# Performance work log

Measured on AMD Instinct MI355X. Metric: run time of the kernel, lower is better.

Reference implementation:

```python
import jax, jax.numpy as jnp
import numpy as np

NUM_HEADS = 16
THETA = 10000.0


def _rope_headaxis(x, cos, sin):
    # x: (B, T, H, D). Faithful to the source module: RoPE angles are
    # indexed by the HEAD axis (the module's view_as_complex bug), with
    # consecutive pairs along D forming (real, imag).
    B, T, H, D = x.shape
    xp = x.reshape(B, T, H, D // 2, 2)
    x0, x1 = xp[..., 0], xp[..., 1]
    # cos/sin: (H, D//2) broadcast over (B, T)
    o0 = x0 * cos - x1 * sin
    o1 = x0 * sin + x1 * cos
    return jnp.stack([o0, o1], axis=-1).reshape(B, T, H, D)


def setup_inputs() -> dict:
    key = jax.random.key(0)
    k1, k2, k3 = jax.random.split(key, 3)
    B, T, C = 2, 2048, 1024
    H = NUM_HEADS
    D = C // H
    KV = 2 * 2048  # kv_seq_len * 2 cache allocation
    x = jax.random.normal(k1, (B, T, C), dtype=jnp.float32)
    w_qkv = jax.random.normal(k2, (3 * C, C), dtype=jnp.float32) * 0.02
    w_out = jax.random.normal(k3, (C, C), dtype=jnp.float32) * 0.02
    cache_k = jnp.zeros((B, KV, H, D), dtype=jnp.float32)
    cache_v = jnp.zeros((B, KV, H, D), dtype=jnp.float32)
    return {"x": x, "w_qkv": w_qkv, "w_out": w_out,
            "cache_k": cache_k, "cache_v": cache_v, "start_pos": 0}


def reference(x, w_qkv, w_out, cache_k, cache_v, start_pos):
    B, T, C = x.shape
    H = NUM_HEADS
    D = C // H
    scale = 1.0 / np.sqrt(D).astype(np.float32)

    qkv = x @ w_qkv.T  # (B, T, 3C)
    q, k, v = jnp.split(qkv, 3, axis=-1)
    q = q.reshape(B, T, H, D)
    k = k.reshape(B, T, H, D)
    v = v.reshape(B, T, H, D)

    # RoPE angles: outer(arange(T), inv_freq) sliced to first H rows
    # (source applies positions along the head axis).
    dim_half = D // 2
    inv_freq = 1.0 / (THETA ** (jnp.arange(dim_half, dtype=jnp.float32) / dim_half))
    angles = jnp.arange(H, dtype=jnp.float32)[:, None] * inv_freq[None, :]  # (H, D/2)
    cos, sin = jnp.cos(angles), jnp.sin(angles)
    q = _rope_headaxis(q, cos, sin)
    k = _rope_headaxis(k, cos, sin)

    end_pos = start_pos + T
    cache_k = cache_k.at[:, start_pos:end_pos].set(jax.lax.stop_gradient(k))
    cache_v = cache_v.at[:, start_pos:end_pos].set(jax.lax.stop_gradient(v))
    k_full = cache_k[:, :end_pos]  # (B, S, H, D)
    v_full = cache_v[:, :end_pos]

    scores = jnp.einsum('bthd,bshd->bhts', q, k_full) * scale  # (B,H,T,S)
    causal = jnp.triu(jnp.ones((T, end_pos), dtype=bool), k=1)
    scores = jnp.where(causal[None, None], -jnp.inf, scores)
    probs = jax.nn.softmax(scores, axis=-1)  # dropout is identity at inference
    ctx = jnp.einsum('bhts,bshd->bthd', probs, v_full).reshape(B, T, C)
    return ctx @ w_out.T
```

## Files before the change

### kernel.cpp

```cpp
#include <hip/hip_runtime.h>
#include <hip/hip_bf16.h>
#include <stdint.h>

typedef __attribute__((ext_vector_type(8))) short short8;
typedef __attribute__((ext_vector_type(4))) float f32x4;

static __device__ __forceinline__ unsigned short f2bf(float f) {
  union { float f; unsigned u; } v; v.f = f;
  return (unsigned short)((v.u + 0x7fffu + ((v.u >> 16) & 1u)) >> 16);
}
static __device__ __forceinline__ float bf2f(unsigned short h) {
  union { unsigned u; float f; } v; v.u = ((unsigned)h) << 16;
  return v.f;
}
static __device__ __forceinline__ unsigned cvt_pk_bf16(float lo, float hi) {
  unsigned r;
  asm("v_cvt_pk_bf16_f32 %0, %1, %2" : "=v"(r) : "v"(lo), "v"(hi));
  return r;
}

#define GLL16(gp, lp) __builtin_amdgcn_global_load_lds(                        \
    (__attribute__((address_space(1))) void*)(uintptr_t)(gp),                  \
    (__attribute__((address_space(3))) void*)(lp), 16, 0, 0)

#define SWZ(r, e) ((e) ^ (((r) & 7) << 3))

__global__ void cast3(const float* __restrict__ a, unsigned short* __restrict__ oa, int na4,
                      const float* __restrict__ b, unsigned short* __restrict__ ob, int nb4,
                      const float* __restrict__ c, unsigned short* __restrict__ oc, int nc4) {
  int i = blockIdx.x * 256 + threadIdx.x;
  const float* src;
  unsigned short* dst;
  int j = i;
  if (j < na4) { src = a; dst = oa; }
  else if ((j -= na4) < nb4) { src = b; dst = ob; }
  else { j -= nb4; if (j >= nc4) return; src = c; dst = oc; }
  const float4 v = reinterpret_cast<const float4*>(src)[j];
  ushort4 o;
  o.x = f2bf(v.x); o.y = f2bf(v.y); o.z = f2bf(v.z); o.w = f2bf(v.w);
  reinterpret_cast<ushort4*>(dst)[j] = o;
}

__global__ __launch_bounds__(256) void gemm_qkv(
    const unsigned short* __restrict__ A, const unsigned short* __restrict__ B,
    unsigned short* __restrict__ qb, unsigned short* __restrict__ kb,
    unsigned short* __restrict__ vt) {
  constexpr int K = 1024;
  __shared__ unsigned short smem[128 * 136];
  const int tid = threadIdx.x;
  const int lane = tid & 63;
  const int w = tid >> 6;
  const int wr = w >> 1, wc = w & 1;
  const int l15 = lane & 15, lg = lane >> 4;
  const size_t bm = (size_t)blockIdx.x * 128;
  const size_t bn = (size_t)blockIdx.y * 128;
  const unsigned short* Ab = A + bm * K;
  const unsigned short* Bb = B + bn * K;
  f32x4 acc[4][4];
#pragma unroll
  for (int m = 0; m < 4; ++m)
#pragma unroll
    for (int n = 0; n < 4; ++n) acc[m][n] = (f32x4){0.f, 0.f, 0.f, 0.f};

#pragma unroll
  for (int p = 0; p < 2; ++p) {
    const int flat = p * 256 + tid;
    const int row = flat >> 2;
    const int c8 = (flat & 3) << 3;
    GLL16(Ab + (size_t)row * K + c8, smem + flat * 8);
    GLL16(Bb + (size_t)row * K + c8, smem + 8192 + flat * 8);
  }
  __syncthreads();
  int cur = 0;
  for (int k0 = 0; k0 < K; k0 += 32) {
    if (k0 + 32 < K) {
      const int nb = cur ^ 1;
#pragma unroll
      for (int p = 0; p < 2; ++p) {
        const int flat = p * 256 + tid;
        const int row = flat >> 2;
        const int c8 = (flat & 3) << 3;
        GLL16(Ab + (size_t)row * K + k0 + 32 + c8, smem + nb * 4096 + flat * 8);
        GLL16(Bb + (size_t)row * K + k0 + 32 + c8, smem + 8192 + nb * 4096 + flat * 8);
      }
    }
    const unsigned short* Asc = smem + cur * 4096;
    const unsigned short* Bsc = smem + 8192 + cur * 4096;
    short8 af[4], bf[4];
#pragma unroll
    for (int m = 0; m < 4; ++m)
      af[m] = *reinterpret_cast<const short8*>(Asc + ((wr * 64 + m * 16 + l15) * 32 + lg * 8));
#pragma unroll
    for (int n = 0; n < 4; ++n)
      bf[n] = *reinterpret_cast<const short8*>(Bsc + ((wc * 64 + n * 16 + l15) * 32 + lg * 8));
#pragma unroll
    for (int m = 0; m < 4; ++m)
#pragma unroll
      for (int n = 0; n < 4; ++n)
        acc[m][n] = __builtin_amdgcn_mfma_f32_16x16x32_bf16(af[m], bf[n], acc[m][n], 0, 0, 0);
    __syncthreads();
    cur ^= 1;
  }

  const int sec = (int)(bn >> 10);
  const int hbase = (int)((bn & 1023) >> 6);
  if (sec < 2) {
    unsigned* st32 = reinterpret_cast<unsigned*>(smem);
    const float scl = sec ? 1.0f : (0.125f * 1.44269504089f);
    const bool even = (l15 & 1) == 0;
#pragma unroll
    for (int n = 0; n < 4; ++n) {
      const int c = wc * 64 + n * 16 + l15;
      const int jj = (c & 63) >> 1;
      const int h = hbase + (c >> 6);
      const float freq = __expf(-(float)jj * (9.210340371976184f / 32.0f));
      float sn, cs;
      __sincosf((float)h * freq, &sn, &cs);
#pragma unroll
      for (int m = 0; m < 4; ++m)
#pragma unroll
        for (int r = 0; r < 4; ++r) {
          const float v = acc[m][n][r];
          const float p = __shfl_xor(v, 1);
          if (even) {
            const float o0 = (v * cs - p * sn) * scl;
            const float o1 = (v * sn + p * cs) * scl;
            const int tl = wr * 64 + lg * 4 + m * 16 + r;
            st32[tl * 68 + (c >> 1)] = cvt_pk_bf16(o0, o1);
          }
        }
    }
    __syncthreads();
    unsigned short* dst = sec ? kb : qb;
#pragma unroll
    for (int p8 = 0; p8 < 8; ++p8) {
      const int id = p8 * 256 + tid;
      const int tlc = id >> 4, cch = id & 15;
      const short8 val = *reinterpret_cast<const short8*>(smem + tlc * 136 + cch * 8);
      const int trow = (int)bm + tlc;
      const int b = trow >> 11, t = trow & 2047;
      const int h = hbase + (cch >> 3), d0 = (cch & 7) * 8;
      *reinterpret_cast<short8*>(dst + (((size_t)(b * 16 + h) * 2048 + t) << 6) + d0) = val;
    }
  } else {
#pragma unroll
    for (int n = 0; n < 4; ++n) {
      const int c = wc * 64 + n * 16 + l15;
      const int x = (c & 7) << 2;
#pragma unroll
      for (int m = 0; m < 4; ++m) {
        const int gt = wr * 16 + lg + m * 4;
        ushort4 pk;
        pk.x = f2bf(acc[m][n][0]); pk.y = f2bf(acc[m][n][1]);
        pk.z = f2bf(acc[m][n][2]); pk.w = f2bf(acc[m][n][3]);
        *reinterpret_cast<ushort4*>(smem + c * 136 + ((gt ^ x) << 2)) = pk;
      }
    }
    __syncthreads();
#pragma unroll
    for (int p8 = 0; p8 < 8; ++p8) {
      const int id = p8 * 256 + tid;
      const int cl = id >> 4, tch = id & 15;
      const int x = (cl & 7) << 2;
      const short8 val =
          *reinterpret_cast<const short8*>(smem + cl * 136 + (((tch * 2) ^ x) << 2));
      const int col = (int)(bn & 1023) + cl;
      const int h = col >> 6, d = col & 63;
      const int trow = (int)bm + tch * 8;
      const int b = trow >> 11, t = trow & 2047;
      *reinterpret_cast<short8*>(vt + ((size_t)((b * 16 + h) * 64 + d)) * 2048 + t) = val;
    }
  }
}

__global__ __launch_bounds__(256) void gemm_nt_f32(
    const unsigned short* __restrict__ A, const unsigned short* __restrict__ B,
    float* __restrict__ Cout, int M, int N, int K) {
  __shared__ unsigned short smem[4 * 4096];
  const int tid = threadIdx.x;
  const int lane = tid & 63;
  const int w = tid >> 6;
  const int wr = w >> 1, wc = w & 1;
  const int l15 = lane & 15, lg = lane >> 4;
  const size_t bm = (size_t)blockIdx.x * 128;
  const size_t bn = (size_t)blockIdx.y * 128;
  const unsigned short* Ab = A + bm * K;
  const unsigned short* Bb = B + bn * K;
  f32x4 acc[4][4];
#pragma unroll
  for (int m = 0; m < 4; ++m)
#pragma unroll
    for (int n = 0; n < 4; ++n) acc[m][n] = (f32x4){0.f, 0.f, 0.f, 0.f};

#pragma unroll
  for (int p = 0; p < 2; ++p) {
    const int flat = p * 256 + tid;
    const int row = flat >> 2;
    const int c8 = (flat & 3) << 3;
    GLL16(Ab + (size_t)row * K + c8, smem + flat * 8);
    GLL16(Bb + (size_t)row * K + c8, smem + 8192 + flat * 8);
  }
  __syncthreads();
  int cur = 0;
  for (int k0 = 0; k0 < K; k0 += 32) {
    if (k0 + 32 < K) {
      const int nb = cur ^ 1;
#pragma unroll
      for (int p = 0; p < 2; ++p) {
        const int flat = p * 256 + tid;
        const int row = flat >> 2;
        const int c8 = (flat & 3) << 3;
        GLL16(Ab + (size_t)row * K + k0 + 32 + c8, smem + nb * 4096 + flat * 8);
        GLL16(Bb + (size_t)row * K + k0 + 32 + c8, smem + 8192 + nb * 4096 + flat * 8);
      }
    }
    const unsigned short* Asc = smem + cur * 4096;
    const unsigned short* Bsc = smem + 8192 + cur * 4096;
    short8 af[4], bf[4];
#pragma unroll
    for (int m = 0; m < 4; ++m)
      af[m] = *reinterpret_cast<const short8*>(Asc + ((wr * 64 + m * 16 + l15) * 32 + lg * 8));
#pragma unroll
    for (int n = 0; n < 4; ++n)
      bf[n] = *reinterpret_cast<const short8*>(Bsc + ((wc * 64 + n * 16 + l15) * 32 + lg * 8));
#pragma unroll
    for (int m = 0; m < 4; ++m)
#pragma unroll
      for (int n = 0; n < 4; ++n)
        acc[m][n] = __builtin_amdgcn_mfma_f32_16x16x32_bf16(af[m], bf[n], acc[m][n], 0, 0, 0);
    __syncthreads();
    cur ^= 1;
  }
  const size_t row0 = bm + wr * 64 + lg * 4;
  const size_t col0 = bn + wc * 64 + l15;
#pragma unroll
  for (int m = 0; m < 4; ++m)
#pragma unroll
    for (int n = 0; n < 4; ++n)
#pragma unroll
      for (int r = 0; r < 4; ++r)
        Cout[(row0 + m * 16 + r) * N + col0 + n * 16] = acc[m][n][r];
}

__global__ __launch_bounds__(256) void attn_kernel(
    const unsigned short* __restrict__ qb, const unsigned short* __restrict__ kb,
    const unsigned short* __restrict__ vt, unsigned short* __restrict__ partO,
    float2* __restrict__ partML) {
  __shared__ unsigned short Ks[2][64 * 64];
  __shared__ unsigned short Vs[2][64 * 64];
  __shared__ unsigned short Ps[4][16 * 64];
  const int tid = threadIdx.x;
  const int lane = tid & 63;
  const int w = tid >> 6;
  const int l15 = lane & 15, lg = lane >> 4;
  const int sx = blockIdx.x & 1, px = blockIdx.x >> 1;
  const int bh = blockIdx.y;
  unsigned short* Pw = &Ps[w][0];

  const unsigned short* kg[2];
  const unsigned short* vg[2];
#pragma unroll
  for (int p = 0; p < 2; ++p) {
    const int f = p * 256 + tid;
    const int row = f >> 3;
    const int gc8 = SWZ(row, (f & 7) << 3);
    kg[p] = kb + ((size_t)bh * 2048 + row) * 64 + gc8;
    vg[p] = vt + ((size_t)bh * 64 + row) * 2048 + gc8;
  }

  int cur = 0;
#pragma unroll 1
  for (int mem = 0; mem < 2; ++mem) {
    const int qt = mem ? (31 - px) : px;
    const int nt = qt + 1;
    const int mid = (nt + 1) >> 1;
    const int sb = sx ? mid : 0;
    const int se = sx ? nt : mid;
    const int nh = se - sb;
    const int qw = qt * 64 + w * 16;
    const unsigned short* Qp = qb + ((size_t)bh * 2048 + qw) * 64;
    const short8 qf0 = *reinterpret_cast<const short8*>(Qp + (size_t)l15 * 64 + lg * 8);
    const short8 qf1 = *reinterpret_cast<const short8*>(Qp + (size_t)l15 * 64 + 32 + lg * 8);
    float mrun = -1e30f, lrun = 0.f;
    f32x4 o[4];
#pragma unroll
    for (int dt = 0; dt < 4; ++dt) o[dt] = (f32x4){0.f, 0.f, 0.f, 0.f};

    if (nh > 0) {
#pragma unroll
      for (int p = 0; p < 2; ++p) {
        const int f = p * 256 + tid;
        GLL16(kg[p] + (size_t)sb * 64 * 64, &Ks[cur][f * 8]);
        GLL16(vg[p] + (size_t)sb * 64, &Vs[cur][f * 8]);
      }
      __syncthreads();

#pragma unroll 1
      for (int it = 0; it < nh; ++it) {
        const int ti = sb + it;
        const int s0 = ti * 64;
        if (it + 1 < nh) {
#pragma unroll
          for (int p = 0; p < 2; ++p) {
            const int f = p * 256 + tid;
            GLL16(kg[p] + (size_t)(ti + 1) * 64 * 64, &Ks[cur ^ 1][f * 8]);
            GLL16(vg[p] + (size_t)(ti + 1) * 64, &Vs[cur ^ 1][f * 8]);
          }
        }
        const unsigned short* Kc = &Ks[cur][0];
        const unsigned short* Vc = &Vs[cur][0];
        f32x4 sc[4];
        __builtin_amdgcn_s_setprio(1);
#pragma unroll
        for (int st = 0; st < 4; ++st) {
          const int kr = st * 16 + l15;
          const short8 kf0 = *reinterpret_cast<const short8*>(Kc + kr * 64 + SWZ(kr, lg * 8));
          const short8 kf1 = *reinterpret_cast<const short8*>(Kc + kr * 64 + SWZ(kr, 32 + lg * 8));
          f32x4 z = (f32x4){0.f, 0.f, 0.f, 0.f};
          z = __builtin_amdgcn_mfma_f32_16x16x32_bf16(kf0, qf0, z, 0, 0, 0);
          z = __builtin_amdgcn_mfma_f32_16x16x32_bf16(kf1, qf1, z, 0, 0, 0);
          sc[st] = z;
        }
        __builtin_amdgcn_s_setprio(0);
        if (s0 + 63 > qw) {
          const int sbase = s0 + lg * 4 - qw - l15;
#pragma unroll
          for (int st = 0; st < 4; ++st)
#pragma unroll
            for (int r = 0; r < 4; ++r)
              if (sbase + st * 16 + r > 0) sc[st][r] = -1e30f;
        }
        float tmax = sc[0][0];
#pragma unroll
        for (int st = 0; st < 4; ++st)
#pragma unroll
          for (int r = 0; r < 4; ++r) tmax = fmaxf(tmax, sc[st][r]);
        tmax = fmaxf(tmax, __shfl_xor(tmax, 16));
        tmax = fmaxf(tmax, __shfl_xor(tmax, 32));
        if (__any(tmax > mrun + 8.f)) {
          const float mn = fmaxf(mrun, tmax);
          const float c = exp2f(mrun - mn);
          mrun = mn;
          lrun *= c;
#pragma unroll
          for (int r = 0; r < 4; ++r) {
            const float cq = __shfl(c, lg * 4 + r);
            o[0][r] *= cq; o[1][r] *= cq; o[2][r] *= cq; o[3][r] *= cq;
          }
        }
        float psum = 0.f;
#pragma unroll
        for (int st = 0; st < 4; ++st) {
          const float p0 = exp2f(sc[st][0] - mrun);
          const float p1 = exp2f(sc[st][1] - mrun);
          const float p2 = exp2f(sc[st][2] - mrun);
          const float p3 = exp2f(sc[st][3] - mrun);
          psum += (p0 + p1) + (p2 + p3);
          const unsigned lo = cvt_pk_bf16(p0, p1);
          const unsigned hi = cvt_pk_bf16(p2, p3);
          const int off = l15 * 64 + SWZ(l15, st * 16 + lg * 4);
          *reinterpret_cast<uint2*>(Pw + off) = make_uint2(lo, hi);
        }
        psum += __shfl_xor(psum, 16);
        psum += __shfl_xor(psum, 32);
        lrun += psum;
        __builtin_amdgcn_s_setprio(1);
#pragma unroll
        for (int sc2 = 0; sc2 < 2; ++sc2) {
          const short8 pf =
              *reinterpret_cast<const short8*>(Pw + l15 * 64 + SWZ(l15, sc2 * 32 + lg * 8));
#pragma unroll
          for (int dt = 0; dt < 4; ++dt) {
            const int vr = dt * 16 + l15;
            const short8 vf =
                *reinterpret_cast<const short8*>(Vc + vr * 64 + SWZ(vr, sc2 * 32 + lg * 8));
            o[dt] = __builtin_amdgcn_mfma_f32_16x16x32_bf16(pf, vf, o[dt], 0, 0, 0);
          }
        }
        __builtin_amdgcn_s_setprio(0);
        __syncthreads();
        cur ^= 1;
      }
    }
#pragma unroll
    for (int r = 0; r < 4; ++r) {
      const int t = qw + lg * 4 + r;
      const size_t base = ((size_t)sx * 65536 + (size_t)bh * 2048 + t) * 64;
#pragma unroll
      for (int dt = 0; dt < 4; ++dt) partO[base + dt * 16 + l15] = f2bf(o[dt][r]);
    }
    if (lg == 0) partML[sx * 65536 + bh * 2048 + qw + l15] = make_float2(mrun, lrun);
  }
}

__global__ __launch_bounds__(256) void attn_combine(
    const unsigned short* __restrict__ partO, const float2* __restrict__ partML,
    unsigned short* __restrict__ ctx) {
  const int id = blockIdx.x * 256 + threadIdx.x;
  const int R = id >> 3;
  const int d8 = (id & 7) << 3;
  const float2 ml0 = partML[R];
  const float2 ml1 = partML[65536 + R];
  const float M = fmaxf(ml0.x, ml1.x);
  const float w0 = exp2f(ml0.x - M), w1 = exp2f(ml1.x - M);
  const float inv = __builtin_amdgcn_rcpf(ml0.y * w0 + ml1.y * w1);
  const short8 a = *reinterpret_cast<const short8*>(partO + ((size_t)R * 64 + d8));
  const short8 c = *reinterpret_cast<const short8*>(partO + ((size_t)(65536 + R) * 64 + d8));
  const int bh = R >> 11, t = R & 2047;
  const int b = bh >> 4, h = bh & 15;
  short8 outv;
#pragma unroll
  for (int e = 0; e < 8; ++e)
    outv[e] = (short)f2bf((bf2f((unsigned short)a[e]) * w0 +
                           bf2f((unsigned short)c[e]) * w1) * inv);
  *reinterpret_cast<short8*>(ctx + ((size_t)(b * 2048 + t) * 1024 + h * 64 + d8)) = outv;
}

extern "C" void kernel_launch(void* const* d_in, const int* in_sizes, int n_in,
                              void* d_out, int out_size, void* d_ws, size_t ws_size,
                              hipStream_t stream) {
  const float* x = (const float*)d_in[0];
  const float* w_qkv = (const float*)d_in[1];
  const float* w_out = (const float*)d_in[2];
  char* ws = (char*)d_ws;
  unsigned short* xb    = (unsigned short*)(ws);
  unsigned short* wqkvb = (unsigned short*)(ws + (8ull  << 20));
  unsigned short* woutb = (unsigned short*)(ws + (14ull << 20));
  unsigned short* partO = (unsigned short*)(ws + (16ull << 20));
  float2* partML        = (float2*)(ws + (32ull << 20));
  unsigned short* q_buf = (unsigned short*)(ws + (40ull << 20));
  unsigned short* k_buf = (unsigned short*)(ws + (48ull << 20));
  unsigned short* vt    = (unsigned short*)(ws + (56ull << 20));
  unsigned short* ctxb  = (unsigned short*)(ws + (64ull << 20));

  cast3<<<8192, 256, 0, stream>>>(x, xb, 1048576, w_qkv, wqkvb, 786432,
                                  w_out, woutb, 262144);
  gemm_qkv<<<dim3(32, 24), 256, 0, stream>>>(xb, wqkvb, q_buf, k_buf, vt);
  attn_kernel<<<dim3(32, 32), 256, 0, stream>>>(q_buf, k_buf, vt, partO, partML);
  attn_combine<<<2048, 256, 0, stream>>>(partO, partML, ctxb);
  gemm_nt_f32<<<dim3(32, 8), 256, 0, stream>>>(ctxb, woutb, (float*)d_out, 4096, 1024, 1024);
}
```

Before: 117.0 us.

## Widen attention blocks to 128 query rows with 8 waves sharing K/V tiles

The attention kernel now launches 512 threads (8 waves), each block covering a 128-row query tile instead of 64, so each K/V tile staged in LDS is reused by twice as many query rows. K/V loading drops from two loads per thread to one, and the causal tile range and query-tile pairing are recomputed for the larger tiles. The running max init changes from -1e30 to -1e5. In exchange, per-block LDS grows and blocks get larger, which may reduce occupancy, and any unseen code that depends on the old tile size must match.

Measured after the change: 148.0 us. +26.4%, slower.

```diff
diff --git a/kernel.cpp b/kernel.cpp
--- a/kernel.cpp
+++ b/kernel.cpp
@@ -242,13 +242,13 @@
         Cout[(row0 + m * 16 + r) * N + col0 + n * 16] = acc[m][n][r];
 }
 
-__global__ __launch_bounds__(256) void attn_kernel(
+__global__ __launch_bounds__(512) void attn_kernel(
     const unsigned short* __restrict__ qb, const unsigned short* __restrict__ kb,
     const unsigned short* __restrict__ vt, unsigned short* __restrict__ partO,
     float2* __restrict__ partML) {
   __shared__ unsigned short Ks[2][64 * 64];
   __shared__ unsigned short Vs[2][64 * 64];
-  __shared__ unsigned short Ps[4][16 * 64];
+  __shared__ unsigned short Ps[8][16 * 64];
   const int tid = threadIdx.x;
   const int lane = tid & 63;
   const int w = tid >> 6;
@@ -257,42 +257,32 @@
   const int bh = blockIdx.y;
   unsigned short* Pw = &Ps[w][0];
 
-  const unsigned short* kg[2];
-  const unsigned short* vg[2];
-#pragma unroll
-  for (int p = 0; p < 2; ++p) {
-    const int f = p * 256 + tid;
-    const int row = f >> 3;
-    const int gc8 = SWZ(row, (f & 7) << 3);
-    kg[p] = kb + ((size_t)bh * 2048 + row) * 64 + gc8;
-    vg[p] = vt + ((size_t)bh * 64 + row) * 2048 + gc8;
-  }
+  const int srow = tid >> 3;
+  const int gc8 = SWZ(srow, (tid & 7) << 3);
+  const unsigned short* kg = kb + ((size_t)bh * 2048 + srow) * 64 + gc8;
+  const unsigned short* vg = vt + ((size_t)bh * 64 + srow) * 2048 + gc8;
 
   int cur = 0;
 #pragma unroll 1
   for (int mem = 0; mem < 2; ++mem) {
-    const int qt = mem ? (31 - px) : px;
-    const int nt = qt + 1;
-    const int mid = (nt + 1) >> 1;
+    const int qt = mem ? (15 - px) : px;
+    const int nt = 2 * qt + 2;
+    const int mid = nt >> 1;
     const int sb = sx ? mid : 0;
     const int se = sx ? nt : mid;
     const int nh = se - sb;
-    const int qw = qt * 64 + w * 16;
+    const int qw = qt * 128 + w * 16;
     const unsigned short* Qp = qb + ((size_t)bh * 2048 + qw) * 64;
     const short8 qf0 = *reinterpret_cast<const short8*>(Qp + (size_t)l15 * 64 + lg * 8);
     const short8 qf1 = *reinterpret_cast<const short8*>(Qp + (size_t)l15 * 64 + 32 + lg * 8);
-    float mrun = -1e30f, lrun = 0.f;
+    float mrun = -1e5f, lrun = 0.f;
     f32x4 o[4];
 #pragma unroll
     for (int dt = 0; dt < 4; ++dt) o[dt] = (f32x4){0.f, 0.f, 0.f, 0.f};
 
     if (nh > 0) {
-#pragma unroll
-      for (int p = 0; p < 2; ++p) {
-        const int f = p * 256 + tid;
-        GLL16(kg[p] + (size_t)sb * 64 * 64, &Ks[cur][f * 8]);
-        GLL16(vg[p] + (size_t)sb * 64, &Vs[cur][f * 8]);
-      }
+      GLL16(kg + (size_t)sb * 4096, &Ks[cur][tid * 8]);
+      GLL16(vg + (size_t)sb * 64, &Vs[cur][tid * 8]);
       __syncthreads();
 
 #pragma unroll 1
@@ -300,12 +290,8 @@
         const int ti = sb + it;
         const int s0 = ti * 64;
         if (it + 1 < nh) {
-#pragma unroll
-          for (int p = 0; p < 2; ++p) {
-            const int f = p * 256 + tid;
-            GLL16(kg[p] + (size_t)(ti + 1) * 64 * 64, &Ks[cur ^ 1][f * 8]);
-            GLL16(vg[p] + (size_t)(ti + 1) * 64, &Vs[cur ^ 1][f * 8]);
-          }
+          GLL16(kg + (size_t)(ti + 1) * 4096, &Ks[cur ^ 1][tid * 8]);
+          GLL16(vg + (size_t)(ti + 1) * 64, &Vs[cur ^ 1][tid * 8]);
         }
         const unsigned short* Kc = &Ks[cur][0];
         const unsigned short* Vc = &Vs[cur][0];
@@ -436,7 +422,7 @@
   cast3<<<8192, 256, 0, stream>>>(x, xb, 1048576, w_qkv, wqkvb, 786432,
                                   w_out, woutb, 262144);
   gemm_qkv<<<dim3(32, 24), 256, 0, stream>>>(xb, wqkvb, q_buf, k_buf, vt);
-  attn_kernel<<<dim3(32, 32), 256, 0, stream>>>(q_buf, k_buf, vt, partO, partML);
+  attn_kernel<<<dim3(32, 32), 512, 0, stream>>>(q_buf, k_buf, vt, partO, partML);
   attn_combine<<<2048, 256, 0, stream>>>(partO, partML, ctxb);
   gemm_nt_f32<<<dim3(32, 8), 256, 0, stream>>>(ctxb, woutb, (float*)d_out, 4096, 1024, 1024);
 }
```

## Double attention query tile per wave and remap blocks for K/V L2 locality

Applied to the files above, without the earlier changes.

Each wave now processes 32 query rows (two 16-row sub-tiles) instead of 16, so each block covers 128 queries. Every K/V tile loaded into LDS is reused across twice as many queries, roughly halving K/V traffic. The grid is halved to 512 blocks, and blockIdx is remapped so neighbouring blocks share the same head. This costs more registers and LDS for P, fewer blocks for occupancy and load balance, and a changed initial running max (-1e5).

Result: no change. 119.4 us (+2.0%).

```diff
diff --git a/kernel.cpp b/kernel.cpp
--- a/kernel.cpp
+++ b/kernel.cpp
@@ -248,22 +248,25 @@
     float2* __restrict__ partML) {
   __shared__ unsigned short Ks[2][64 * 64];
   __shared__ unsigned short Vs[2][64 * 64];
-  __shared__ unsigned short Ps[4][16 * 64];
+  __shared__ unsigned short Ps[4][32 * 64];
   const int tid = threadIdx.x;
   const int lane = tid & 63;
   const int w = tid >> 6;
   const int l15 = lane & 15, lg = lane >> 4;
-  const int sx = blockIdx.x & 1, px = blockIdx.x >> 1;
-  const int bh = blockIdx.y;
+  const int fid = (int)(blockIdx.y * 16 + blockIdx.x);
+  const int j = fid >> 3;
+  const int bh = ((fid & 7) << 2) + (j >> 4);
+  const int inner = j & 15;
+  const int sx = inner & 1, px = inner >> 1;
   unsigned short* Pw = &Ps[w][0];
 
   const unsigned short* kg[2];
   const unsigned short* vg[2];
 #pragma unroll
   for (int p = 0; p < 2; ++p) {
-    const int f = p * 256 + tid;
-    const int row = f >> 3;
-    const int gc8 = SWZ(row, (f & 7) << 3);
+    const int flat = p * 256 + tid;
+    const int row = flat >> 3;
+    const int gc8 = SWZ(row, (flat & 7) << 3);
     kg[p] = kb + ((size_t)bh * 2048 + row) * 64 + gc8;
     vg[p] = vt + ((size_t)bh * 64 + row) * 2048 + gc8;
   }
@@ -271,27 +274,33 @@
   int cur = 0;
 #pragma unroll 1
   for (int mem = 0; mem < 2; ++mem) {
-    const int qt = mem ? (31 - px) : px;
-    const int nt = qt + 1;
-    const int mid = (nt + 1) >> 1;
+    const int qt = mem ? (15 - px) : px;
+    const int nt = 2 * qt + 2;
+    const int mid = nt >> 1;
     const int sb = sx ? mid : 0;
     const int se = sx ? nt : mid;
     const int nh = se - sb;
-    const int qw = qt * 64 + w * 16;
+    const int qw = qt * 128 + w * 32;
     const unsigned short* Qp = qb + ((size_t)bh * 2048 + qw) * 64;
-    const short8 qf0 = *reinterpret_cast<const short8*>(Qp + (size_t)l15 * 64 + lg * 8);
-    const short8 qf1 = *reinterpret_cast<const short8*>(Qp + (size_t)l15 * 64 + 32 + lg * 8);
-    float mrun = -1e30f, lrun = 0.f;
-    f32x4 o[4];
-#pragma unroll
-    for (int dt = 0; dt < 4; ++dt) o[dt] = (f32x4){0.f, 0.f, 0.f, 0.f};
+    short8 qf[2][2];
+#pragma unroll
+    for (int qs = 0; qs < 2; ++qs) {
+      qf[qs][0] = *reinterpret_cast<const short8*>(Qp + (size_t)(qs * 16 + l15) * 64 + lg * 8);
+      qf[qs][1] = *reinterpret_cast<const short8*>(Qp + (size_t)(qs * 16 + l15) * 64 + 32 + lg * 8);
+    }
+    float mrun[2] = {-1e5f, -1e5f}, lrun[2] = {0.f, 0.f};
+    f32x4 o[2][4];
+#pragma unroll
+    for (int qs = 0; qs < 2; ++qs)
+#pragma unroll
+      for (int dt = 0; dt < 4; ++dt) o[qs][dt] = (f32x4){0.f, 0.f, 0.f, 0.f};
 
     if (nh > 0) {
 #pragma unroll
       for (int p = 0; p < 2; ++p) {
-        const int f = p * 256 + tid;
-        GLL16(kg[p] + (size_t)sb * 64 * 64, &Ks[cur][f * 8]);
-        GLL16(vg[p] + (size_t)sb * 64, &Vs[cur][f * 8]);
+        const int flat = p * 256 + tid;
+        GLL16(kg[p] + (size_t)sb * 4096, &Ks[cur][flat * 8]);
+        GLL16(vg[p] + (size_t)sb * 64, &Vs[cur][flat * 8]);
       }
       __syncthreads();
 
@@ -302,79 +311,92 @@
         if (it + 1 < nh) {
 #pragma unroll
           for (int p = 0; p < 2; ++p) {
-            const int f = p * 256 + tid;
-            GLL16(kg[p] + (size_t)(ti + 1) * 64 * 64, &Ks[cur ^ 1][f * 8]);
-            GLL16(vg[p] + (size_t)(ti + 1) * 64, &Vs[cur ^ 1][f * 8]);
+            const int flat = p * 256 + tid;
+            GLL16(kg[p] + (size_t)(ti + 1) * 4096, &Ks[cur ^ 1][flat * 8]);
+            GLL16(vg[p] + (size_t)(ti + 1) * 64, &Vs[cur ^ 1][flat * 8]);
           }
         }
         const unsigned short* Kc = &Ks[cur][0];
         const unsigned short* Vc = &Vs[cur][0];
-        f32x4 sc[4];
+        f32x4 sc[2][4];
         __builtin_amdgcn_s_setprio(1);
 #pragma unroll
         for (int st = 0; st < 4; ++st) {
           const int kr = st * 16 + l15;
           const short8 kf0 = *reinterpret_cast<const short8*>(Kc + kr * 64 + SWZ(kr, lg * 8));
           const short8 kf1 = *reinterpret_cast<const short8*>(Kc + kr * 64 + SWZ(kr, 32 + lg * 8));
-          f32x4 z = (f32x4){0.f, 0.f, 0.f, 0.f};
-          z = __builtin_amdgcn_mfma_f32_16x16x32_bf16(kf0, qf0, z, 0, 0, 0);
-          z = __builtin_amdgcn_mfma_f32_16x16x32_bf16(kf1, qf1, z, 0, 0, 0);
-          sc[st] = z;
+#pragma unroll
+          for (int qs = 0; qs < 2; ++qs) {
+            f32x4 z = (f32x4){0.f, 0.f, 0.f, 0.f};
+            z = __builtin_amdgcn_mfma_f32_16x16x32_bf16(kf0, qf[qs][0], z, 0, 0, 0);
+            z = __builtin_amdgcn_mfma_f32_16x16x32_bf16(kf1, qf[qs][1], z, 0, 0, 0);
+            sc[qs][st] = z;
+          }
         }
         __builtin_amdgcn_s_setprio(0);
-        if (s0 + 63 > qw) {
-          const int sbase = s0 + lg * 4 - qw - l15;
+#pragma unroll
+        for (int qs = 0; qs < 2; ++qs) {
+          if (s0 + 63 > qw + qs * 16) {
+            const int sbase = s0 + lg * 4 - (qw + qs * 16) - l15;
+#pragma unroll
+            for (int st = 0; st < 4; ++st)
+#pragma unroll
+              for (int r = 0; r < 4; ++r)
+                if (sbase + st * 16 + r > 0) sc[qs][st][r] = -1e30f;
+          }
+        }
+#pragma unroll
+        for (int qs = 0; qs < 2; ++qs) {
+          float tmax = sc[qs][0][0];
 #pragma unroll
           for (int st = 0; st < 4; ++st)
 #pragma unroll
-            for (int r = 0; r < 4; ++r)
-              if (sbase + st * 16 + r > 0) sc[st][r] = -1e30f;
-        }
-        float tmax = sc[0][0];
-#pragma unroll
-        for (int st = 0; st < 4; ++st)
-#pragma unroll
-          for (int r = 0; r < 4; ++r) tmax = fmaxf(tmax, sc[st][r]);
-        tmax = fmaxf(tmax, __shfl_xor(tmax, 16));
-        tmax = fmaxf(tmax, __shfl_xor(tmax, 32));
-        if (__any(tmax > mrun + 8.f)) {
-          const float mn = fmaxf(mrun, tmax);
-          const float c = exp2f(mrun - mn);
-          mrun = mn;
-          lrun *= c;
-#pragma unroll
-          for (int r = 0; r < 4; ++r) {
-            const float cq = __shfl(c, lg * 4 + r);
-            o[0][r] *= cq; o[1][r] *= cq; o[2][r] *= cq; o[3][r] *= cq;
-          }
-        }
-        float psum = 0.f;
-#pragma unroll
-        for (int st = 0; st < 4; ++st) {
-          const float p0 = exp2f(sc[st][0] - mrun);
-          const float p1 = exp2f(sc[st][1] - mrun);
-          const float p2 = exp2f(sc[st][2] - mrun);
-          const float p3 = exp2f(sc[st][3] - mrun);
-          psum += (p0 + p1) + (p2 + p3);
-          const unsigned lo = cvt_pk_bf16(p0, p1);
-          const unsigned hi = cvt_pk_bf16(p2, p3);
-          const int off = l15 * 64 + SWZ(l15, st * 16 + lg * 4);
-          *reinterpret_cast<uint2*>(Pw + off) = make_uint2(lo, hi);
-        }
-        psum += __shfl_xor(psum, 16);
-        psum += __shfl_xor(psum, 32);
-        lrun += psum;
+            for (int r = 0; r < 4; ++r) tmax = fmaxf(tmax, sc[qs][st][r]);
+          tmax = fmaxf(tmax, __shfl_xor(tmax, 16));
+          tmax = fmaxf(tmax, __shfl_xor(tmax, 32));
+          if (__any(tmax > mrun[qs] + 8.f)) {
+            const float mn = fmaxf(mrun[qs], tmax);
+            const float c = exp2f(mrun[qs] - mn);
+            mrun[qs] = mn;
+            lrun[qs] *= c;
+#pragma unroll
+            for (int r = 0; r < 4; ++r) {
+              const float cq = __shfl(c, lg * 4 + r);
+              o[qs][0][r] *= cq; o[qs][1][r] *= cq;
+              o[qs][2][r] *= cq; o[qs][3][r] *= cq;
+            }
+          }
+          float psum = 0.f;
+#pragma unroll
+          for (int st = 0; st < 4; ++st) {
+            const float p0 = exp2f(sc[qs][st][0] - mrun[qs]);
+            const float p1 = exp2f(sc[qs][st][1] - mrun[qs]);
+            const float p2 = exp2f(sc[qs][st][2] - mrun[qs]);
+            const float p3 = exp2f(sc[qs][st][3] - mrun[qs]);
+            psum += (p0 + p1) + (p2 + p3);
+            const unsigned lo = cvt_pk_bf16(p0, p1);
+            const unsigned hi = cvt_pk_bf16(p2, p3);
+            const int off = qs * 1024 + l15 * 64 + SWZ(l15, st * 16 + lg * 4);
+            *reinterpret_cast<uint2*>(Pw + off) = make_uint2(lo, hi);
+          }
+          psum += __shfl_xor(psum, 16);
+          psum += __shfl_xor(psum, 32);
+          lrun[qs] += psum;
+        }
         __builtin_amdgcn_s_setprio(1);
 #pragma unroll
         for (int sc2 = 0; sc2 < 2; ++sc2) {
-          const short8 pf =
-              *reinterpret_cast<const short8*>(Pw + l15 * 64 + SWZ(l15, sc2 * 32 + lg * 8));
+          const short8 pf0 = *reinterpret_cast<const short8*>(
+              Pw + l15 * 64 + SWZ(l15, sc2 * 32 + lg * 8));
+          const short8 pf1 = *reinterpret_cast<const short8*>(
+              Pw + 1024 + l15 * 64 + SWZ(l15, sc2 * 32 + lg * 8));
 #pragma unroll
           for (int dt = 0; dt < 4; ++dt) {
             const int vr = dt * 16 + l15;
             const short8 vf =
                 *reinterpret_cast<const short8*>(Vc + vr * 64 + SWZ(vr, sc2 * 32 + lg * 8));
-            o[dt] = __builtin_amdgcn_mfma_f32_16x16x32_bf16(pf, vf, o[dt], 0, 0, 0);
+            o[0][dt] = __builtin_amdgcn_mfma_f32_16x16x32_bf16(pf0, vf, o[0][dt], 0, 0, 0);
+            o[1][dt] = __builtin_amdgcn_mfma_f32_16x16x32_bf16(pf1, vf, o[1][dt], 0, 0, 0);
           }
         }
         __builtin_amdgcn_s_setprio(0);
@@ -383,13 +405,18 @@
       }
     }
 #pragma unroll
-    for (int r = 0; r < 4; ++r) {
-      const int t = qw + lg * 4 + r;
-      const size_t base = ((size_t)sx * 65536 + (size_t)bh * 2048 + t) * 64;
-#pragma unroll
-      for (int dt = 0; dt < 4; ++dt) partO[base + dt * 16 + l15] = f2bf(o[dt][r]);
-    }
-    if (lg == 0) partML[sx * 65536 + bh * 2048 + qw + l15] = make_float2(mrun, lrun);
+    for (int qs = 0; qs < 2; ++qs) {
+#pragma unroll
+      for (int r = 0; r < 4; ++r) {
+        const int t = qw + qs * 16 + lg * 4 + r;
+        const size_t base = ((size_t)sx * 65536 + (size_t)bh * 2048 + t) * 64;
+#pragma unroll
+        for (int dt = 0; dt < 4; ++dt) partO[base + dt * 16 + l15] = f2bf(o[qs][dt][r]);
+      }
+      if (lg == 0)
+        partML[sx * 65536 + bh * 2048 + qw + qs * 16 + l15] =
+            make_float2(mrun[qs], lrun[qs]);
+    }
   }
 }
 
@@ -436,7 +463,7 @@
   cast3<<<8192, 256, 0, stream>>>(x, xb, 1048576, w_qkv, wqkvb, 786432,
                                   w_out, woutb, 262144);
   gemm_qkv<<<dim3(32, 24), 256, 0, stream>>>(xb, wqkvb, q_buf, k_buf, vt);
-  attn_kernel<<<dim3(32, 32), 256, 0, stream>>>(q_buf, k_buf, vt, partO, partML);
+  attn_kernel<<<dim3(16, 32), 256, 0, stream>>>(q_buf, k_buf, vt, partO, partML);
   attn_combine<<<2048, 256, 0, stream>>>(partO, partML, ctxb);
   gemm_nt_f32<<<dim3(32, 8), 256, 0, stream>>>(ctxb, woutb, (float*)d_out, 4096, 1024, 1024);
 }
```
